# Performance work log

Measured on AMD Instinct MI355X. Metric: run time of the kernel, lower is better.

## Reference

```python
import jax, jax.numpy as jnp
import numpy as np

H = 8
D_MODEL = 512
D_K = D_MODEL // H


def setup_inputs() -> dict:
    key = jax.random.key(0)
    ks = jax.random.split(key, 11)
    B, S = 4, 2048
    sc = 1.0 / np.sqrt(D_MODEL)
    inp = {
        "q": jax.random.normal(ks[0], (B, S, D_MODEL), jnp.float32),
        "k": jax.random.normal(ks[1], (B, S, D_MODEL), jnp.float32),
        "v": jax.random.normal(ks[2], (B, S, D_MODEL), jnp.float32),
        "Wq": jax.random.normal(ks[3], (D_MODEL, D_MODEL), jnp.float32) * sc,
        "bq": jnp.zeros((D_MODEL,), jnp.float32),
        "Wk": jax.random.normal(ks[4], (D_MODEL, D_MODEL), jnp.float32) * sc,
        "bk": jnp.zeros((D_MODEL,), jnp.float32),
        "Wv": jax.random.normal(ks[5], (D_MODEL, D_MODEL), jnp.float32) * sc,
        "bv": jnp.zeros((D_MODEL,), jnp.float32),
        "Wo": jax.random.normal(ks[6], (D_MODEL, D_MODEL), jnp.float32) * sc,
        "bo": jnp.zeros((D_MODEL,), jnp.float32),
    }
    return inp


def reference(q, k, v, Wq, bq, Wk, bk, Wv, bv, Wo, bo):
    B, S, _ = q.shape
    # Linear projections, then split heads: [B, S, D] -> [B, H, S, d_k]
    def split_heads(x):
        return x.reshape(B, S, H, D_K).transpose(0, 2, 1, 3)
    qh = split_heads(q @ Wq + bq)
    kh = split_heads(k @ Wk + bk)
    vh = split_heads(v @ Wv + bv)
    # scores: [B, H, S, S]
    scores = jnp.einsum("bhqd,bhkd->bhqk", qh, kh) / jnp.sqrt(jnp.float32(D_K))
    attn = jax.nn.softmax(scores, axis=-1)  # dropout p=0.0 -> identity
    out = jnp.einsum("bhqk,bhkd->bhqd", attn, vh)
    concat = out.transpose(0, 2, 1, 3).reshape(B, S, D_MODEL)
    return concat @ Wo + bo
```

## Files before the change

### kernel.cpp

```cpp
#include <hip/hip_runtime.h>

#define LOG2E 1.4426950408889634f

typedef __attribute__((ext_vector_type(4))) float  f32x4;
typedef __attribute__((ext_vector_type(8))) __bf16 bf16x8;
typedef __attribute__((ext_vector_type(8))) short  sh8;
typedef __attribute__((ext_vector_type(4))) short  sh4;

__device__ __forceinline__ short f2bf(float f) {
  union { float f; unsigned u; } x; x.f = f;
  unsigned r = (x.u + 0x7fffu + ((x.u >> 16) & 1u)) >> 16;
  return (short)r;
}

__global__ __launch_bounds__(256)
void wtrans(const float* __restrict__ Wq, const float* __restrict__ Wk,
            const float* __restrict__ Wv, const float* __restrict__ Wo,
            short* __restrict__ WqT, short* __restrict__ WkT,
            short* __restrict__ WvT, short* __restrict__ WoT)
{
  const float* W; short* WT;
  switch (blockIdx.z) {
    case 0:  W = Wq; WT = WqT; break;
    case 1:  W = Wk; WT = WkT; break;
    case 2:  W = Wv; WT = WvT; break;
    default: W = Wo; WT = WoT; break;
  }
  __shared__ float ts[32][33];
  const int t = threadIdx.x;
  const int k0 = blockIdx.x * 32, n0 = blockIdx.y * 32;
  const int r = t >> 3, c4 = (t & 7) * 4;
  float4 v = *(const float4*)&W[(size_t)(k0 + r) * 512 + n0 + c4];
  ts[r][c4 + 0] = v.x; ts[r][c4 + 1] = v.y; ts[r][c4 + 2] = v.z; ts[r][c4 + 3] = v.w;
  __syncthreads();
  sh4 o;
  o[0] = f2bf(ts[c4 + 0][r]); o[1] = f2bf(ts[c4 + 1][r]);
  o[2] = f2bf(ts[c4 + 2][r]); o[3] = f2bf(ts[c4 + 3][r]);
  *(sh4*)&WT[(size_t)(n0 + r) * 512 + k0 + c4] = o;
}

template<bool A_F32, bool B_F32, int OMODE>
__global__ __launch_bounds__(256)
void gemm512(const void* __restrict__ Ap, const void* __restrict__ Bp,
             const float* __restrict__ bias, void* __restrict__ outp)
{
  __shared__ short As[128][72];
  __shared__ short Bs[128][72];
  const int rm = blockIdx.x * 128, cn = blockIdx.y * 128;
  const int tid = threadIdx.x, l = tid & 63, wid = tid >> 6;
  const int wr = wid >> 1, wc = wid & 1;
  const int lr = l & 15, lk = (l >> 4) * 8, lj = (l >> 4) * 4;
  const int sr = tid >> 1, sc = (tid & 1) * 32;

  f32x4 acc[4][4];
  const f32x4 z4 = {0.f, 0.f, 0.f, 0.f};
  #pragma unroll
  for (int i = 0; i < 4; ++i)
    #pragma unroll
    for (int j = 0; j < 4; ++j) acc[i][j] = z4;

  for (int k0 = 0; k0 < 512; k0 += 64) {
    if constexpr (A_F32) {
      const float* A = (const float*)Ap + (size_t)(rm + sr) * 512 + k0 + sc;
      #pragma unroll
      for (int g = 0; g < 4; ++g) {
        float4 f0 = ((const float4*)A)[2 * g];
        float4 f1 = ((const float4*)A)[2 * g + 1];
        sh8 s;
        s[0] = f2bf(f0.x); s[1] = f2bf(f0.y); s[2] = f2bf(f0.z); s[3] = f2bf(f0.w);
        s[4] = f2bf(f1.x); s[5] = f2bf(f1.y); s[6] = f2bf(f1.z); s[7] = f2bf(f1.w);
        *(sh8*)&As[sr][sc + 8 * g] = s;
      }
    } else {
      const short* A = (const short*)Ap + (size_t)(rm + sr) * 512 + k0 + sc;
      #pragma unroll
      for (int g = 0; g < 4; ++g)
        *(sh8*)&As[sr][sc + 8 * g] = ((const sh8*)A)[g];
    }
    if constexpr (B_F32) {
      const float* B = (const float*)Bp + (size_t)(cn + sr) * 512 + k0 + sc;
      #pragma unroll
      for (int g = 0; g < 4; ++g) {
        float4 f0 = ((const float4*)B)[2 * g];
        float4 f1 = ((const float4*)B)[2 * g + 1];
        sh8 s;
        s[0] = f2bf(f0.x); s[1] = f2bf(f0.y); s[2] = f2bf(f0.z); s[3] = f2bf(f0.w);
        s[4] = f2bf(f1.x); s[5] = f2bf(f1.y); s[6] = f2bf(f1.z); s[7] = f2bf(f1.w);
        *(sh8*)&Bs[sr][sc + 8 * g] = s;
      }
    } else {
      const short* B = (const short*)Bp + (size_t)(cn + sr) * 512 + k0 + sc;
      #pragma unroll
      for (int g = 0; g < 4; ++g)
        *(sh8*)&Bs[sr][sc + 8 * g] = ((const sh8*)B)[g];
    }
    __syncthreads();
    #pragma unroll
    for (int kk = 0; kk < 2; ++kk) {
      bf16x8 af[4], bfr[4];
      #pragma unroll
      for (int mi = 0; mi < 4; ++mi)
        af[mi] = *(const bf16x8*)&As[wr * 64 + mi * 16 + lr][kk * 32 + lk];
      #pragma unroll
      for (int ni = 0; ni < 4; ++ni)
        bfr[ni] = *(const bf16x8*)&Bs[wc * 64 + ni * 16 + lr][kk * 32 + lk];
      #pragma unroll
      for (int mi = 0; mi < 4; ++mi)
        #pragma unroll
        for (int ni = 0; ni < 4; ++ni)
          acc[mi][ni] = __builtin_amdgcn_mfma_f32_16x16x32_bf16(af[mi], bfr[ni], acc[mi][ni], 0, 0, 0);
    }
    __syncthreads();
  }

  #pragma unroll
  for (int mi = 0; mi < 4; ++mi) {
    #pragma unroll
    for (int ni = 0; ni < 4; ++ni) {
      const int row = rm + wr * 64 + mi * 16 + lj;
      const int col = cn + wc * 64 + ni * 16 + lr;
      if constexpr (OMODE == 2) {
        float* out = (float*)outp;
        const float bv = bias[col];
        #pragma unroll
        for (int j = 0; j < 4; ++j)
          out[(size_t)(row + j) * 512 + col] = acc[mi][ni][j] + bv;
      } else if constexpr (OMODE == 0) {
        short* out = (short*)outp;
        const float bv = bias[col];
        const int h = col >> 6, d = col & 63;
        #pragma unroll
        for (int j = 0; j < 4; ++j) {
          const int R = row + j, b = R >> 11, s = R & 2047;
          out[(((size_t)(b * 8 + h)) * 2048 + s) * 64 + d] = f2bf(acc[mi][ni][j] + bv);
        }
      } else {
        short* out = (short*)outp;
        const int b = col >> 11, s = col & 2047;
        #pragma unroll
        for (int j = 0; j < 4; ++j) {
          const int mr = row + j;
          const int h = mr >> 6, d = mr & 63;
          out[(((size_t)(b * 8 + h)) * 64 + d) * 2048 + s] = f2bf(acc[mi][ni][j] + bias[mr]);
        }
      }
    }
  }
}

__global__ __launch_bounds__(256)
void attn(const short* __restrict__ Qh, const short* __restrict__ Kh,
          const short* __restrict__ VhT, short* __restrict__ Cc)
{
  __shared__ short Ks[64][72];
  __shared__ short Vs[64][72];
  __shared__ short Ps[4][32][72];

  const int qt = blockIdx.x, bh = blockIdx.y;
  const int tid = threadIdx.x, l = tid & 63, w = tid >> 6;
  const int lr = l & 15, lk = (l >> 4) * 8, lj = (l >> 4) * 4;
  const int q0 = qt * 128 + w * 32;

  const short* Qb = Qh + (size_t)bh * 2048 * 64;
  const short* Kb = Kh + (size_t)bh * 2048 * 64;
  const short* Vb = VhT + (size_t)bh * 64 * 2048;

  bf16x8 aq[2][2];
  #pragma unroll
  for (int mi = 0; mi < 2; ++mi)
    #pragma unroll
    for (int kk = 0; kk < 2; ++kk)
      aq[mi][kk] = *(const bf16x8*)&Qb[(size_t)(q0 + mi * 16 + lr) * 64 + kk * 32 + lk];

  const f32x4 z4 = {0.f, 0.f, 0.f, 0.f};
  f32x4 accO[2][4];
  float mrun[2][4], lrun[2][4];
  #pragma unroll
  for (int mi = 0; mi < 2; ++mi) {
    #pragma unroll
    for (int ni = 0; ni < 4; ++ni) accO[mi][ni] = z4;
    #pragma unroll
    for (int j = 0; j < 4; ++j) { mrun[mi][j] = -1e30f; lrun[mi][j] = 0.f; }
  }

  const int str = tid >> 2, stc = (tid & 3) * 16;

  for (int kv = 0; kv < 2048; kv += 64) {
    {
      const sh8* ksrc = (const sh8*)&Kb[(size_t)(kv + str) * 64 + stc];
      *(sh8*)&Ks[str][stc]     = ksrc[0];
      *(sh8*)&Ks[str][stc + 8] = ksrc[1];
      const sh8* vsrc = (const sh8*)&Vb[(size_t)str * 2048 + kv + stc];
      *(sh8*)&Vs[str][stc]     = vsrc[0];
      *(sh8*)&Vs[str][stc + 8] = vsrc[1];
    }
    __syncthreads();

    f32x4 accS[2][4];
    #pragma unroll
    for (int mi = 0; mi < 2; ++mi)
      #pragma unroll
      for (int ni = 0; ni < 4; ++ni) accS[mi][ni] = z4;
    #pragma unroll
    for (int kk = 0; kk < 2; ++kk) {
      bf16x8 bk[4];
      #pragma unroll
      for (int ni = 0; ni < 4; ++ni)
        bk[ni] = *(const bf16x8*)&Ks[ni * 16 + lr][kk * 32 + lk];
      #pragma unroll
      for (int mi = 0; mi < 2; ++mi)
        #pragma unroll
        for (int ni = 0; ni < 4; ++ni)
          accS[mi][ni] = __builtin_amdgcn_mfma_f32_16x16x32_bf16(aq[mi][kk], bk[ni], accS[mi][ni], 0, 0, 0);
    }

    #pragma unroll
    for (int mi = 0; mi < 2; ++mi) {
      #pragma unroll
      for (int j = 0; j < 4; ++j) {
        float s0 = accS[mi][0][j] * 0.125f, s1 = accS[mi][1][j] * 0.125f;
        float s2 = accS[mi][2][j] * 0.125f, s3 = accS[mi][3][j] * 0.125f;
        float mx = fmaxf(fmaxf(s0, s1), fmaxf(s2, s3));
        mx = fmaxf(mx, __shfl_xor(mx, 1));
        mx = fmaxf(mx, __shfl_xor(mx, 2));
        mx = fmaxf(mx, __shfl_xor(mx, 4));
        mx = fmaxf(mx, __shfl_xor(mx, 8));
        const float mnew = fmaxf(mrun[mi][j], mx);
        const float corr = __builtin_amdgcn_exp2f((mrun[mi][j] - mnew) * LOG2E);
        mrun[mi][j] = mnew;
        const float p0 = __builtin_amdgcn_exp2f((s0 - mnew) * LOG2E);
        const float p1 = __builtin_amdgcn_exp2f((s1 - mnew) * LOG2E);
        const float p2 = __builtin_amdgcn_exp2f((s2 - mnew) * LOG2E);
        const float p3 = __builtin_amdgcn_exp2f((s3 - mnew) * LOG2E);
        float ps = p0 + p1 + p2 + p3;
        ps += __shfl_xor(ps, 1);
        ps += __shfl_xor(ps, 2);
        ps += __shfl_xor(ps, 4);
        ps += __shfl_xor(ps, 8);
        lrun[mi][j] = lrun[mi][j] * corr + ps;
        #pragma unroll
        for (int ni = 0; ni < 4; ++ni) accO[mi][ni][j] *= corr;
        const int pr = mi * 16 + lj + j;
        Ps[w][pr][0 * 16 + lr] = f2bf(p0);
        Ps[w][pr][1 * 16 + lr] = f2bf(p1);
        Ps[w][pr][2 * 16 + lr] = f2bf(p2);
        Ps[w][pr][3 * 16 + lr] = f2bf(p3);
      }
    }

    asm volatile("s_waitcnt lgkmcnt(0)" ::: "memory");
    __builtin_amdgcn_sched_barrier(0);

    #pragma unroll
    for (int kk = 0; kk < 2; ++kk) {
      bf16x8 bv[4];
      #pragma unroll
      for (int ni = 0; ni < 4; ++ni)
        bv[ni] = *(const bf16x8*)&Vs[ni * 16 + lr][kk * 32 + lk];
      #pragma unroll
      for (int mi = 0; mi < 2; ++mi) {
        bf16x8 pa = *(const bf16x8*)&Ps[w][mi * 16 + lr][kk * 32 + lk];
        #pragma unroll
        for (int ni = 0; ni < 4; ++ni)
          accO[mi][ni] = __builtin_amdgcn_mfma_f32_16x16x32_bf16(pa, bv[ni], accO[mi][ni], 0, 0, 0);
      }
    }
    __syncthreads();
  }

  const int b = bh >> 3, h = bh & 7;
  #pragma unroll
  for (int mi = 0; mi < 2; ++mi) {
    #pragma unroll
    for (int j = 0; j < 4; ++j) {
      const float inv = 1.0f / lrun[mi][j];
      const int s = q0 + mi * 16 + lj + j;
      #pragma unroll
      for (int ni = 0; ni < 4; ++ni) {
        const int d = ni * 16 + lr;
        Cc[((size_t)(b * 2048 + s)) * 512 + h * 64 + d] = f2bf(accO[mi][ni][j] * inv);
      }
    }
  }
}

extern "C" void kernel_launch(void* const* d_in, const int* in_sizes, int n_in,
                              void* d_out, int out_size, void* d_ws, size_t ws_size,
                              hipStream_t stream)
{
  const float* q  = (const float*)d_in[0];
  const float* k  = (const float*)d_in[1];
  const float* v  = (const float*)d_in[2];
  const float* Wq = (const float*)d_in[3];
  const float* bq = (const float*)d_in[4];
  const float* Wk = (const float*)d_in[5];
  const float* bk = (const float*)d_in[6];
  const float* Wv = (const float*)d_in[7];
  const float* bv = (const float*)d_in[8];
  const float* Wo = (const float*)d_in[9];
  const float* bo = (const float*)d_in[10];
  float* out = (float*)d_out;

  char* ws = (char*)d_ws;
  short* WqT = (short*)(ws + 0 * 524288);
  short* WkT = (short*)(ws + 1 * 524288);
  short* WvT = (short*)(ws + 2 * 524288);
  short* WoT = (short*)(ws + 3 * 524288);
  short* Qh  = (short*)(ws + 4 * 524288);
  short* Kh  = (short*)(ws + 4 * 524288 + 1 * 8388608);
  short* VhT = (short*)(ws + 4 * 524288 + 2 * 8388608);
  short* Cc  = (short*)(ws + 4 * 524288 + 3 * 8388608);

  wtrans<<<dim3(16, 16, 4), 256, 0, stream>>>(Wq, Wk, Wv, Wo, WqT, WkT, WvT, WoT);
  gemm512<true,  false, 0><<<dim3(64, 4), 256, 0, stream>>>(q, WqT, bq, Qh);
  gemm512<true,  false, 0><<<dim3(64, 4), 256, 0, stream>>>(k, WkT, bk, Kh);
  gemm512<false, true,  1><<<dim3(4, 64), 256, 0, stream>>>(WvT, v, bv, VhT);
  attn<<<dim3(16, 32), 256, 0, stream>>>(Qh, Kh, VhT, Cc);
  gemm512<false, false, 2><<<dim3(64, 4), 256, 0, stream>>>(Cc, WoT, bo, out);
}
```

Baseline: 297.7 us.

## Halve attention query tile per block and fold softmax scale into Q

Each wave in the attention kernel now handles 16 query rows instead of 32, so a block covers 64 queries and the grid doubles to 1024 blocks. This spreads work across more CUs and lowers register pressure. The price is that each K/V tile loaded into shared memory is reused by half as many queries, which doubles K/V global traffic. The 1/sqrt(dk)*log2e scale is also folded into Q once at load time, which removes the per-score multiplies but rounds the scaled Q to bf16.

```diff
diff --git a/kernel.cpp b/kernel.cpp
--- a/kernel.cpp
+++ b/kernel.cpp
@@ -154,34 +154,37 @@
 {
   __shared__ short Ks[64][72];
   __shared__ short Vs[64][72];
-  __shared__ short Ps[4][32][72];
+  __shared__ short Ps[4][16][80];
 
   const int qt = blockIdx.x, bh = blockIdx.y;
   const int tid = threadIdx.x, l = tid & 63, w = tid >> 6;
   const int lr = l & 15, lk = (l >> 4) * 8, lj = (l >> 4) * 4;
-  const int q0 = qt * 128 + w * 32;
+  const int q0 = qt * 64 + w * 16;
 
   const short* Qb = Qh + (size_t)bh * 2048 * 64;
   const short* Kb = Kh + (size_t)bh * 2048 * 64;
   const short* Vb = VhT + (size_t)bh * 64 * 2048;
 
-  bf16x8 aq[2][2];
-  #pragma unroll
-  for (int mi = 0; mi < 2; ++mi)
-    #pragma unroll
-    for (int kk = 0; kk < 2; ++kk)
-      aq[mi][kk] = *(const bf16x8*)&Qb[(size_t)(q0 + mi * 16 + lr) * 64 + kk * 32 + lk];
+  const float SC = 0.125f * LOG2E;
+  bf16x8 aq[2];
+  #pragma unroll
+  for (int kk = 0; kk < 2; ++kk) {
+    bf16x8 f = *(const bf16x8*)&Qb[(size_t)(q0 + lr) * 64 + kk * 32 + lk];
+    #pragma unroll
+    for (int e = 0; e < 8; ++e) {
+      float x = (float)f[e] * SC;
+      f[e] = (__bf16)x;
+    }
+    aq[kk] = f;
+  }
 
   const f32x4 z4 = {0.f, 0.f, 0.f, 0.f};
-  f32x4 accO[2][4];
-  float mrun[2][4], lrun[2][4];
-  #pragma unroll
-  for (int mi = 0; mi < 2; ++mi) {
-    #pragma unroll
-    for (int ni = 0; ni < 4; ++ni) accO[mi][ni] = z4;
-    #pragma unroll
-    for (int j = 0; j < 4; ++j) { mrun[mi][j] = -1e30f; lrun[mi][j] = 0.f; }
-  }
+  f32x4 accO[4];
+  float mrun[4], lrun[4];
+  #pragma unroll
+  for (int ni = 0; ni < 4; ++ni) accO[ni] = z4;
+  #pragma unroll
+  for (int j = 0; j < 4; ++j) { mrun[j] = -1e30f; lrun[j] = 0.f; }
 
   const int str = tid >> 2, stc = (tid & 3) * 16;
 
@@ -196,11 +199,9 @@
     }
     __syncthreads();
 
-    f32x4 accS[2][4];
-    #pragma unroll
-    for (int mi = 0; mi < 2; ++mi)
-      #pragma unroll
-      for (int ni = 0; ni < 4; ++ni) accS[mi][ni] = z4;
+    f32x4 accS[4];
+    #pragma unroll
+    for (int ni = 0; ni < 4; ++ni) accS[ni] = z4;
     #pragma unroll
     for (int kk = 0; kk < 2; ++kk) {
       bf16x8 bk[4];
@@ -208,44 +209,38 @@
       for (int ni = 0; ni < 4; ++ni)
         bk[ni] = *(const bf16x8*)&Ks[ni * 16 + lr][kk * 32 + lk];
       #pragma unroll
-      for (int mi = 0; mi < 2; ++mi)
-        #pragma unroll
-        for (int ni = 0; ni < 4; ++ni)
-          accS[mi][ni] = __builtin_amdgcn_mfma_f32_16x16x32_bf16(aq[mi][kk], bk[ni], accS[mi][ni], 0, 0, 0);
-    }
-
-    #pragma unroll
-    for (int mi = 0; mi < 2; ++mi) {
-      #pragma unroll
-      for (int j = 0; j < 4; ++j) {
-        float s0 = accS[mi][0][j] * 0.125f, s1 = accS[mi][1][j] * 0.125f;
-        float s2 = accS[mi][2][j] * 0.125f, s3 = accS[mi][3][j] * 0.125f;
-        float mx = fmaxf(fmaxf(s0, s1), fmaxf(s2, s3));
-        mx = fmaxf(mx, __shfl_xor(mx, 1));
-        mx = fmaxf(mx, __shfl_xor(mx, 2));
-        mx = fmaxf(mx, __shfl_xor(mx, 4));
-        mx = fmaxf(mx, __shfl_xor(mx, 8));
-        const float mnew = fmaxf(mrun[mi][j], mx);
-        const float corr = __builtin_amdgcn_exp2f((mrun[mi][j] - mnew) * LOG2E);
-        mrun[mi][j] = mnew;
-        const float p0 = __builtin_amdgcn_exp2f((s0 - mnew) * LOG2E);
-        const float p1 = __builtin_amdgcn_exp2f((s1 - mnew) * LOG2E);
-        const float p2 = __builtin_amdgcn_exp2f((s2 - mnew) * LOG2E);
-        const float p3 = __builtin_amdgcn_exp2f((s3 - mnew) * LOG2E);
-        float ps = p0 + p1 + p2 + p3;
-        ps += __shfl_xor(ps, 1);
-        ps += __shfl_xor(ps, 2);
-        ps += __shfl_xor(ps, 4);
-        ps += __shfl_xor(ps, 8);
-        lrun[mi][j] = lrun[mi][j] * corr + ps;
-        #pragma unroll
-        for (int ni = 0; ni < 4; ++ni) accO[mi][ni][j] *= corr;
-        const int pr = mi * 16 + lj + j;
-        Ps[w][pr][0 * 16 + lr] = f2bf(p0);
-        Ps[w][pr][1 * 16 + lr] = f2bf(p1);
-        Ps[w][pr][2 * 16 + lr] = f2bf(p2);
-        Ps[w][pr][3 * 16 + lr] = f2bf(p3);
-      }
+      for (int ni = 0; ni < 4; ++ni)
+        accS[ni] = __builtin_amdgcn_mfma_f32_16x16x32_bf16(aq[kk], bk[ni], accS[ni], 0, 0, 0);
+    }
+
+    #pragma unroll
+    for (int j = 0; j < 4; ++j) {
+      float s0 = accS[0][j], s1 = accS[1][j], s2 = accS[2][j], s3 = accS[3][j];
+      float mx = fmaxf(fmaxf(s0, s1), fmaxf(s2, s3));
+      mx = fmaxf(mx, __shfl_xor(mx, 1));
+      mx = fmaxf(mx, __shfl_xor(mx, 2));
+      mx = fmaxf(mx, __shfl_xor(mx, 4));
+      mx = fmaxf(mx, __shfl_xor(mx, 8));
+      const float mnew = fmaxf(mrun[j], mx);
+      const float corr = __builtin_amdgcn_exp2f(mrun[j] - mnew);
+      mrun[j] = mnew;
+      const float p0 = __builtin_amdgcn_exp2f(s0 - mnew);
+      const float p1 = __builtin_amdgcn_exp2f(s1 - mnew);
+      const float p2 = __builtin_amdgcn_exp2f(s2 - mnew);
+      const float p3 = __builtin_amdgcn_exp2f(s3 - mnew);
+      float ps = p0 + p1 + p2 + p3;
+      ps += __shfl_xor(ps, 1);
+      ps += __shfl_xor(ps, 2);
+      ps += __shfl_xor(ps, 4);
+      ps += __shfl_xor(ps, 8);
+      lrun[j] = lrun[j] * corr + ps;
+      #pragma unroll
+      for (int ni = 0; ni < 4; ++ni) accO[ni][j] *= corr;
+      const int pr = lj + j;
+      Ps[w][pr][0 * 16 + lr] = f2bf(p0);
+      Ps[w][pr][1 * 16 + lr] = f2bf(p1);
+      Ps[w][pr][2 * 16 + lr] = f2bf(p2);
+      Ps[w][pr][3 * 16 + lr] = f2bf(p3);
     }
 
     asm volatile("s_waitcnt lgkmcnt(0)" ::: "memory");
@@ -257,29 +252,23 @@
       #pragma unroll
       for (int ni = 0; ni < 4; ++ni)
         bv[ni] = *(const bf16x8*)&Vs[ni * 16 + lr][kk * 32 + lk];
-      #pragma unroll
-      for (int mi = 0; mi < 2; ++mi) {
-        bf16x8 pa = *(const bf16x8*)&Ps[w][mi * 16 + lr][kk * 32 + lk];
-        #pragma unroll
-        for (int ni = 0; ni < 4; ++ni)
-          accO[mi][ni] = __builtin_amdgcn_mfma_f32_16x16x32_bf16(pa, bv[ni], accO[mi][ni], 0, 0, 0);
-      }
+      bf16x8 pa = *(const bf16x8*)&Ps[w][lr][kk * 32 + lk];
+      #pragma unroll
+      for (int ni = 0; ni < 4; ++ni)
+        accO[ni] = __builtin_amdgcn_mfma_f32_16x16x32_bf16(pa, bv[ni], accO[ni], 0, 0, 0);
     }
     __syncthreads();
   }
 
   const int b = bh >> 3, h = bh & 7;
   #pragma unroll
-  for (int mi = 0; mi < 2; ++mi) {
-    #pragma unroll
-    for (int j = 0; j < 4; ++j) {
-      const float inv = 1.0f / lrun[mi][j];
-      const int s = q0 + mi * 16 + lj + j;
-      #pragma unroll
-      for (int ni = 0; ni < 4; ++ni) {
-        const int d = ni * 16 + lr;
-        Cc[((size_t)(b * 2048 + s)) * 512 + h * 64 + d] = f2bf(accO[mi][ni][j] * inv);
-      }
+  for (int j = 0; j < 4; ++j) {
+    const float inv = 1.0f / lrun[j];
+    const int s = q0 + lj + j;
+    #pragma unroll
+    for (int ni = 0; ni < 4; ++ni) {
+      const int d = ni * 16 + lr;
+      Cc[((size_t)(b * 2048 + s)) * 512 + h * 64 + d] = f2bf(accO[ni][j] * inv);
     }
   }
 }
@@ -315,6 +304,6 @@
   gemm512<true,  false, 0><<<dim3(64, 4), 256, 0, stream>>>(q, WqT, bq, Qh);
   gemm512<true,  false, 0><<<dim3(64, 4), 256, 0, stream>>>(k, WkT, bk, Kh);
   gemm512<false, true,  1><<<dim3(4, 64), 256, 0, stream>>>(WvT, v, bv, VhT);
-  attn<<<dim3(16, 32), 256, 0, stream>>>(Qh, Kh, VhT, Cc);
+  attn<<<dim3(32, 32), 256, 0, stream>>>(Qh, Kh, VhT, Cc);
   gemm512<false, false, 2><<<dim3(64, 4), 256, 0, stream>>>(Cc, WoT, bo, out);
 }
```

Result: no change. 300.6 us (+1.0%).
